# Kernel tuning notes

Hardware: AMD Instinct MI355X
Metric: run time of the kernel (lower is better)

## Reference

```python
import jax, jax.numpy as jnp
from jax import lax
import numpy as np

CHUNK = 64      # chunk_size init kwarg
MAX_LOG = 20.0  # clamp bound used in ssd()
DT_BIAS = 0.01
NEG_SLOPE = 0.01  # torch LeakyReLU default


def segsum(a):
    """a: (..., T) -> (..., T, T); ss[i,j] = sum_{k=j+1..i} a[k], -inf above diag."""
    T = a.shape[-1]
    rep = jnp.broadcast_to(a[..., :, None], a.shape + (T,))
    strict_lower = jnp.tril(jnp.ones((T, T), dtype=bool), -1)
    ss = jnp.cumsum(jnp.where(strict_lower, rep, 0.0), axis=-2)
    keep = jnp.tril(jnp.ones((T, T), dtype=bool), 0)
    return jnp.where(keep, ss, -jnp.inf)


def setup_inputs() -> dict:
    key = jax.random.key(0)
    ks = jax.random.split(key, 7)
    T, B, S, F = 4096, 4, 16, 64   # time, batch, spatial heads, in_channels
    N, P, K = 16, 64, 5            # state_dim, head_dim, conv_size
    CH = 2 * N + P + 1             # bc_conv out channels = 97
    return {
        "x": jax.random.normal(ks[0], (T, B, S, F), dtype=jnp.float32),
        "conv_w": jax.random.normal(ks[1], (CH, F, K), dtype=jnp.float32) * 0.05,
        "conv_b": jax.random.normal(ks[2], (CH,), dtype=jnp.float32) * 0.05,
        "pass_w": jax.random.normal(ks[3], (1, F), dtype=jnp.float32) * 0.1,
        "pass_b": jax.random.normal(ks[4], (1,), dtype=jnp.float32) * 0.1,
        "red_w": jax.random.normal(ks[5], (1, P), dtype=jnp.float32) * 0.1,
        "red_b": jax.random.normal(ks[6], (1,), dtype=jnp.float32) * 0.1,
        "dt_param": jnp.zeros((1,), dtype=jnp.float32),  # torch init [0.0]
    }


def _forward(x, conv_w, conv_b, pass_w, pass_b, red_w, red_b, dt_param):
    T, B, S, F = x.shape
    CH, _, K = conv_w.shape
    P = red_w.shape[1]
    N = (CH - P - 1) // 2
    c = T // CHUNK

    # ---- _compute_ssm_params (parallel mode, causal left-pad) ----
    xr = jnp.moveaxis(x.reshape(T, B * S, F), 0, 2)          # (bs, F, T)
    xp = jnp.pad(xr, ((0, 0), (0, 0), (K - 1, 0)))           # left pad context
    bcax = lax.conv_general_dilated(
        xp, conv_w, window_strides=(1,), padding="VALID",
        dimension_numbers=("NCH", "OIH", "NCH")) + conv_b[None, :, None]
    bcax = jax.nn.sigmoid(bcax) + bcax                        # (bs, CH, T)
    bcax = bcax.reshape(B, S, CH, T)
    Bm = bcax[:, :, :N, :]                                    # (b,s,n,t)
    Cm = bcax[:, :, N:2 * N, :]                               # (b,s,n,t)
    A = -jnp.abs(bcax[:, :, 2 * N, :])                        # (b,s,t)
    Xc = bcax[:, :, 2 * N + 1:, :]                            # (b,s,p,t)
    dt = jax.nn.softplus(dt_param)[0] + DT_BIAS
    lAd = dt * A                                              # (b,s,t)
    Bd = Bm * ((jnp.exp(lAd) - 1.0) / (A + 1e-9))[:, :, None, :]
    Dx = x @ pass_w[0] + pass_b[0]                            # (t,b,s) passthrough

    # ---- ssd: chunked Mamba-2 scan ----
    Xb = jnp.moveaxis(Xc, 3, 0).swapaxes(0, 1).reshape(B, c, CHUNK, S, P)
    Bb = jnp.moveaxis(Bd, 3, 0).swapaxes(0, 1).reshape(B, c, CHUNK, S, N)
    Cb = jnp.moveaxis(Cm, 3, 0).swapaxes(0, 1).reshape(B, c, CHUNK, S, N)
    Ab = lAd.reshape(B, S, c, CHUNK)                          # (b,s,c,l)
    A_cumsum = jnp.cumsum(Ab, axis=-1)                        # (b,s,c,l)

    L = jnp.exp(jnp.clip(segsum(Ab), -MAX_LOG, MAX_LOG))      # (b,s,c,l,l)
    Y_diag = jnp.einsum("bclsn,bcmsn,bsclm,bcmsp->bclsp", Cb, Bb, L, Xb)

    decay_states = jnp.exp(jnp.clip(A_cumsum[..., -1:] - A_cumsum, -MAX_LOG, MAX_LOG))
    states = jnp.einsum("bclsn,bscl,bclsp->bcspn", Bb, decay_states, Xb)
    states = jnp.concatenate([jnp.zeros_like(states[:, :1]), states], axis=1)

    A_last = jnp.pad(A_cumsum[..., -1], ((0, 0), (0, 0), (1, 0)))  # (b,s,c+1)
    decay_chunk = jnp.exp(jnp.clip(segsum(A_last), -MAX_LOG, MAX_LOG))
    new_states = jnp.einsum("bszc,bcspn->bzspn", decay_chunk, states)
    states_c = new_states[:, :-1]                             # (b,c,s,p,n)

    state_decay_out = jnp.exp(A_cumsum)                       # (b,s,c,l), no clamp (as in source)
    Y_off = jnp.einsum("bclsn,bcspn,bscl->bclsp", Cb, states_c, state_decay_out)

    Y = (Y_diag + Y_off).reshape(B, T, S, P).swapaxes(0, 1)   # (t,b,s,p)

    # ---- reduce + leaky-relu passthrough ----
    y = Y @ red_w[0] + red_b[0]                               # (t,b,s)
    return y + jnp.where(Dx >= 0, Dx, NEG_SLOPE * Dx)


def reference(x, conv_w, conv_b, pass_w, pass_b, red_w, red_b, dt_param):
    return _forward(x, conv_w, conv_b, pass_w, pass_b, red_w, red_b, dt_param)
```

## Files before the change

### kernel.cpp

```cpp
#include <hip/hip_runtime.h>
#include <hip/hip_bf16.h>
#include <math.h>


#define Tn 4096
#define BSn 64
#define Fn 64
#define CHn 97
#define CHP 112
#define Kn 5
#define Nn 16
#define NCn 64

typedef __attribute__((ext_vector_type(8))) short bf16x8;
typedef __attribute__((ext_vector_type(4))) float f32x4;

static __device__ __forceinline__ unsigned short f2bf(float v) {
    __hip_bfloat16 b = __float2bfloat16(v);
    return *reinterpret_cast<unsigned short*>(&b);
}
static __device__ __forceinline__ float bf2f(unsigned short u) {
    unsigned v = ((unsigned)u) << 16;
    return __builtin_bit_cast(float, v);
}

#define OFF_BD   0
#define OFF_CM   (OFF_BD + 4194304)
#define OFF_LAD  (OFF_CM + 4194304)
#define OFF_XQ   (OFF_LAD + 262144)
#define OFF_DL   (OFF_XQ + 262144)
#define OFF_ACS  (OFF_DL + 262144)
#define OFF_SRED (OFF_ACS + 262144)
#define OFF_CSUM (OFF_SRED + 65536)
#define OFF_SNS  (OFF_CSUM + 4096)
#define OFF_WBH  (OFF_SNS + 65536)
#define OFF_WBL  (OFF_WBH + 17920)

__global__ __launch_bounds__(256) void k_prep(const float* __restrict__ conv_w,
                                              const float* __restrict__ pass_w,
                                              unsigned short* __restrict__ wbh,
                                              unsigned short* __restrict__ wbl) {
    int idx = blockIdx.x * 256 + threadIdx.x;
    if (idx >= Kn * CHP * Fn) return;
    int f = idx & 63;
    int rest = idx >> 6;
    int ch = rest % CHP;
    int k = rest / CHP;
    float w = 0.f;
    if (ch < CHn) w = conv_w[(ch * Fn + f) * Kn + k];
    else if (ch == 97 && k == 4) w = pass_w[f];
    unsigned short hi = f2bf(w);
    wbh[idx] = hi;
    if (ch >= 32 && ch < 48)
        wbl[(k * 16 + (ch - 32)) * 64 + f] = f2bf(w - bf2f(hi));
}

__global__ __launch_bounds__(256) void k_fwd(
    const float* __restrict__ x, const unsigned short* __restrict__ wbh,
    const unsigned short* __restrict__ wbl,
    const float* __restrict__ conv_b, const float* __restrict__ pass_b,
    const float* __restrict__ red_w, const float* __restrict__ red_b,
    const float* __restrict__ dtp,
    float* __restrict__ Cm_t, float* __restrict__ Acs_ws,
    float* __restrict__ yp_ws, float* __restrict__ sred_ws,
    float* __restrict__ csum_ws) {
    const int ci = blockIdx.x, bs = blockIdx.y;
    const int tid = threadIdx.x;
    const int wv = tid >> 6, lane = tid & 63;
    const int qd = lane >> 4, n = lane & 15;

    __shared__ alignas(16) unsigned char pool[19584];
    unsigned short* xsb = (unsigned short*)pool;
    unsigned short* xlo = (unsigned short*)(pool + 9792);
    float* B0  = (float*)pool;
    float* Ct  = (float*)(pool + 5120);
    float* pxl = (float*)(pool + 10240);
    float* px2 = (float*)(pool + 11264);
    float* zsh = (float*)(pool + 12288);
    float* dl  = (float*)(pool + 12544);

    const int tB = (wv == 3) ? 6 : wv + 4;
    const unsigned short* pBw = (wv == 2) ? wbl : wbh;
    const int sB = (wv == 2) ? 16 : CHP;
    const int cB = (wv == 2) ? 0 : 16 * tB;
    bf16x8 wA[10], wB[10];
#pragma unroll
    for (int s = 0; s < 10; ++s) {
        const int k = s >> 1, f0 = 32 * (s & 1) + qd * 8;
        wA[s] = *(const bf16x8*)&wbh[((k * CHP + 16 * wv + n) << 6) + f0];
        wB[s] = *(const bf16x8*)&pBw[((k * sB + cB + n) << 6) + f0];
    }

    float4 v[5];
#pragma unroll
    for (int it = 0; it < 5; ++it) {
        int idx = tid + it * 256;
        int tt = idx >> 4, fq = (idx & 15) * 4;
        int t = ci * 64 - 4 + tt;
        v[it] = (idx < 68 * 16 && t >= 0)
                    ? *(const float4*)&x[(t * 64 + bs) * 64 + fq]
                    : make_float4(0.f, 0.f, 0.f, 0.f);
    }
#pragma unroll
    for (int it = 0; it < 5; ++it) {
        int idx = tid + it * 256;
        if (idx < 68 * 16) {
            int tt = idx >> 4, fq = (idx & 15) * 4;
            ushort4 h, lo;
            h.x = f2bf(v[it].x); lo.x = f2bf(v[it].x - bf2f(h.x));
            h.y = f2bf(v[it].y); lo.y = f2bf(v[it].y - bf2f(h.y));
            h.z = f2bf(v[it].z); lo.z = f2bf(v[it].z - bf2f(h.z));
            h.w = f2bf(v[it].w); lo.w = f2bf(v[it].w - bf2f(h.w));
            *(ushort4*)&xsb[tt * 72 + fq] = h;
            *(ushort4*)&xlo[tt * 72 + fq] = lo;
        }
    }
    __syncthreads();

    f32x4 accA[4], accB[4];
#pragma unroll
    for (int rg = 0; rg < 4; ++rg) {
        accA[rg] = (f32x4){0.f, 0.f, 0.f, 0.f};
        accB[rg] = (f32x4){0.f, 0.f, 0.f, 0.f};
    }
    if (wv == 2) {
#pragma unroll
        for (int s = 0; s < 10; ++s) {
            const int k = s >> 1, f0 = 32 * (s & 1) + qd * 8;
#pragma unroll
            for (int rg = 0; rg < 4; ++rg) {
                bf16x8 av = *(const bf16x8*)&xsb[(16 * rg + n + k) * 72 + f0];
                bf16x8 al = *(const bf16x8*)&xlo[(16 * rg + n + k) * 72 + f0];
                accA[rg] = __builtin_amdgcn_mfma_f32_16x16x32_bf16(av, wA[s], accA[rg], 0, 0, 0);
                accA[rg] = __builtin_amdgcn_mfma_f32_16x16x32_bf16(al, wA[s], accA[rg], 0, 0, 0);
                accA[rg] = __builtin_amdgcn_mfma_f32_16x16x32_bf16(av, wB[s], accA[rg], 0, 0, 0);
            }
        }
    } else {
#pragma unroll
        for (int s = 0; s < 10; ++s) {
            const int k = s >> 1, f0 = 32 * (s & 1) + qd * 8;
#pragma unroll
            for (int rg = 0; rg < 4; ++rg) {
                bf16x8 av = *(const bf16x8*)&xsb[(16 * rg + n + k) * 72 + f0];
                accA[rg] = __builtin_amdgcn_mfma_f32_16x16x32_bf16(av, wA[s], accA[rg], 0, 0, 0);
                accB[rg] = __builtin_amdgcn_mfma_f32_16x16x32_bf16(av, wB[s], accB[rg], 0, 0, 0);
            }
        }
    }
    __syncthreads();

    const int cbase = (bs * 64 + ci) * 64;
    float px[4][4];
#pragma unroll
    for (int rg = 0; rg < 4; ++rg)
#pragma unroll
        for (int reg = 0; reg < 4; ++reg) px[rg][reg] = 0.f;

    if (wv == 0) {
        const float cb0 = conv_b[n];
        const float cb4 = conv_b[64 + n], rw4 = red_w[31 + n];
#pragma unroll
        for (int rg = 0; rg < 4; ++rg)
#pragma unroll
            for (int reg = 0; reg < 4; ++reg) {
                int row = 16 * rg + 4 * qd + reg;
                float z0 = accA[rg][reg] + cb0;
                float a0 = z0 + 1.f / (1.f + __expf(-z0));
                accA[rg][reg] = a0;
                B0[row * 20 + n] = a0;
                float z4 = accB[rg][reg] + cb4;
                px[rg][reg] = (z4 + 1.f / (1.f + __expf(-z4))) * rw4;
            }
    } else if (wv == 1) {
        const float cb1 = conv_b[16 + n];
        const float cb5 = conv_b[80 + n], rw5 = red_w[47 + n];
#pragma unroll
        for (int rg = 0; rg < 4; ++rg)
#pragma unroll
            for (int reg = 0; reg < 4; ++reg) {
                int row = 16 * rg + 4 * qd + reg;
                float z1 = accA[rg][reg] + cb1;
                float a1 = z1 + 1.f / (1.f + __expf(-z1));
                Ct[row * 20 + n] = a1;
                Cm_t[(cbase + row) * 16 + n] = a1;
                float z5 = accB[rg][reg] + cb5;
                px[rg][reg] = (z5 + 1.f / (1.f + __expf(-z5))) * rw5;
            }
    } else if (wv == 2) {
        const float cb2 = conv_b[32 + n];
        const float rw2 = (n >= 1) ? red_w[n - 1] : 0.f;
#pragma unroll
        for (int rg = 0; rg < 4; ++rg)
#pragma unroll
            for (int reg = 0; reg < 4; ++reg) {
                int row = 16 * rg + 4 * qd + reg;
                if (n == 0) zsh[row] = accA[rg][reg];
                float z = accA[rg][reg] + cb2;
                px[rg][reg] = (z + 1.f / (1.f + __expf(-z))) * rw2;
            }
    } else {
        const float cb3 = conv_b[48 + n], rw3 = red_w[15 + n];
        const float cb6 = conv_b[96], rw6 = red_w[63];
        const float pb = pass_b[0], rb = red_b[0];
#pragma unroll
        for (int rg = 0; rg < 4; ++rg)
#pragma unroll
            for (int reg = 0; reg < 4; ++reg) {
                int row = 16 * rg + 4 * qd + reg;
                float z3 = accA[rg][reg] + cb3;
                px[rg][reg] = (z3 + 1.f / (1.f + __expf(-z3))) * rw3;
                if (n == 0) {
                    float z6 = accB[rg][reg] + cb6;
                    px[rg][reg] += (z6 + 1.f / (1.f + __expf(-z6))) * rw6;
                }
                if (n == 1) {
                    float Dx = accB[rg][reg] + pb;
                    float DL = (Dx >= 0.f) ? Dx : 0.01f * Dx;
                    dl[row] = DL + rb;
                }
            }
    }
#pragma unroll
    for (int m = 1; m < 16; m <<= 1)
#pragma unroll
        for (int rg = 0; rg < 4; ++rg)
#pragma unroll
            for (int reg = 0; reg < 4; ++reg)
                px[rg][reg] += __shfl_xor(px[rg][reg], m, 64);
    if (n == 0)
#pragma unroll
        for (int rg = 0; rg < 4; ++rg)
#pragma unroll
            for (int reg = 0; reg < 4; ++reg)
                pxl[wv * 64 + 16 * rg + 4 * qd + reg] = px[rg][reg];
    __syncthreads();

    const int l = lane;
    const float dt = log1pf(expf(dtp[0])) + 0.01f;
    float zA = zsh[l] + conv_b[32];
    float aA = zA + 1.f / (1.f + __expf(-zA));
    float An = -fabsf(aA);
    float lAd = dt * An;
    float fac = (__expf(lAd) - 1.f) / (An + 1e-9f);
    float s = lAd;
#pragma unroll
    for (int k = 1; k < 64; k <<= 1) {
        float t = __shfl_up(s, k, 64);
        if (l >= k) s += t;
    }
    const float acs_l = s;
    const float tot = __shfl(s, 63, 64);
    float xq = pxl[0 * 64 + l] + pxl[1 * 64 + l] + pxl[2 * 64 + l] + pxl[3 * 64 + l];
    const float wd = fac * xq;
    const float wsd = wd * __expf(fmaxf(tot - acs_l, -20.f));
    if (wv == 3) {
        Acs_ws[bs * Tn + ci * 64 + l] = acs_l;
        if (l == 0) csum_ws[bs * 64 + ci] = tot;
    }

    const float4 cc0 = *(const float4*)&Ct[l * 20 + 0];
    const float4 cc1 = *(const float4*)&Ct[l * 20 + 4];
    const float4 cc2 = *(const float4*)&Ct[l * 20 + 8];
    const float4 cc3 = *(const float4*)&Ct[l * 20 + 12];
    float part = 0.f;
#pragma unroll
    for (int mm = 0; mm < 16; ++mm) {
        const int m = 16 * wv + mm;
        const float4 b0 = *(const float4*)&B0[m * 20 + 0];
        const float4 b1 = *(const float4*)&B0[m * 20 + 4];
        const float4 b2 = *(const float4*)&B0[m * 20 + 8];
        const float4 b3 = *(const float4*)&B0[m * 20 + 12];
        float g = cc0.x * b0.x + cc0.y * b0.y + cc0.z * b0.z + cc0.w * b0.w +
                  cc1.x * b1.x + cc1.y * b1.y + cc1.z * b1.z + cc1.w * b1.w +
                  cc2.x * b2.x + cc2.y * b2.y + cc2.z * b2.z + cc2.w * b2.w +
                  cc3.x * b3.x + cc3.y * b3.y + cc3.z * b3.z + cc3.w * b3.w;
        float am = __shfl(acs_l, m, 64);
        float wm = __shfl(wd, m, 64);
        float arg = (m <= l) ? fmaxf(acs_l - am, -20.f) : -20.f;
        part += __expf(arg) * g * wm;
    }
    px2[wv * 64 + l] = part;

    if (wv == 0) {
        float sp = 0.f;
#pragma unroll
        for (int rg = 0; rg < 4; ++rg)
#pragma unroll
            for (int reg = 0; reg < 4; ++reg)
                sp += accA[rg][reg] * __shfl(wsd, 16 * rg + 4 * qd + reg, 64);
        sp += __shfl_xor(sp, 16, 64);
        sp += __shfl_xor(sp, 32, 64);
        if (l < 16) sred_ws[(bs * 64 + ci) * 16 + l] = sp;
    }
    __syncthreads();

    if (wv == 0)
        yp_ws[bs * Tn + ci * 64 + l] =
            px2[0 * 64 + l] + px2[1 * 64 + l] + px2[2 * 64 + l] + px2[3 * 64 + l] + dl[l];
}

__global__ __launch_bounds__(256) void k_scan(const float* __restrict__ sred_ws,
                                              const float* __restrict__ csum_ws,
                                              float* __restrict__ sns_ws) {
    const int wid = blockIdx.x * 4 + (threadIdx.x >> 6);
    const int ci = threadIdx.x & 63;
    const int bs = wid >> 4, n = wid & 15;
    float s = sred_ws[(bs * 64 + ci) * 16 + n];
    float d = __expf(csum_ws[bs * 64 + ci]);
#pragma unroll
    for (int k = 1; k < 64; k <<= 1) {
        float dp = __shfl_up(d, k, 64);
        float sp = __shfl_up(s, k, 64);
        if (ci >= k) {
            s = d * sp + s;
            d = d * dp;
        }
    }
    float se = __shfl_up(s, 1, 64);
    sns_ws[(bs * 64 + ci) * 16 + n] = (ci == 0) ? 0.f : se;
}

__global__ __launch_bounds__(256) void k_out(
    const float* __restrict__ Cm_t, const float* __restrict__ Acs_ws,
    const float* __restrict__ sns_ws, const float* __restrict__ yp_ws,
    float* __restrict__ out) {
    const int bs = blockIdx.y;
    const int tid = threadIdx.x;
    const int wv = tid >> 6, l = tid & 63;
    const int ci = blockIdx.x * 4 + wv;
    __shared__ float sn[4][16];
    const int base = bs * Tn + ci * 64;

    if (l < 16) sn[wv][l] = sns_ws[(bs * 64 + ci) * 16 + l];
    const float4* crow = (const float4*)&Cm_t[((bs * 64 + ci) * 64 + l) * 16];
    float4 c0 = crow[0], c1 = crow[1], c2 = crow[2], c3 = crow[3];
    float yp = yp_ws[base + l];
    float acl = Acs_ws[base + l];
    __syncthreads();

    const float* s = sn[wv];
    float go = c0.x * s[0] + c0.y * s[1] + c0.z * s[2] + c0.w * s[3] +
               c1.x * s[4] + c1.y * s[5] + c1.z * s[6] + c1.w * s[7] +
               c2.x * s[8] + c2.y * s[9] + c2.z * s[10] + c2.w * s[11] +
               c3.x * s[12] + c3.y * s[13] + c3.z * s[14] + c3.w * s[15];
    out[(ci * 64 + l) * 64 + bs] = yp + __expf(acl) * go;
}

extern "C" void kernel_launch(void* const* d_in, const int* in_sizes, int n_in,
                              void* d_out, int out_size, void* d_ws,
                              size_t ws_size, hipStream_t stream) {
    const float* x = (const float*)d_in[0];
    const float* conv_w = (const float*)d_in[1];
    const float* conv_b = (const float*)d_in[2];
    const float* pass_w = (const float*)d_in[3];
    const float* pass_b = (const float*)d_in[4];
    const float* red_w = (const float*)d_in[5];
    const float* red_b = (const float*)d_in[6];
    const float* dtp = (const float*)d_in[7];
    float* out = (float*)d_out;
    float* W = (float*)d_ws;
    (void)in_sizes; (void)n_in; (void)out_size; (void)ws_size;

    float* Cm_t = W + OFF_CM;
    float* yp_ws = W + OFF_DL;
    float* Acs_ws = W + OFF_ACS;
    float* sred_ws = W + OFF_SRED;
    float* csum_ws = W + OFF_CSUM;
    float* sns_ws = W + OFF_SNS;
    unsigned short* wbh = (unsigned short*)(W + OFF_WBH);
    unsigned short* wbl = (unsigned short*)(W + OFF_WBL);

    k_prep<<<dim3((Kn * CHP * Fn + 255) / 256), dim3(256), 0, stream>>>(
        conv_w, pass_w, wbh, wbl);
    k_fwd<<<dim3(NCn, BSn), dim3(256), 0, stream>>>(
        x, wbh, wbl, conv_b, pass_b, red_w, red_b, dtp,
        Cm_t, Acs_ws, yp_ws, sred_ws, csum_ws);
    k_scan<<<dim3(256), dim3(256), 0, stream>>>(sred_ws, csum_ws, sns_ws);
    k_out<<<dim3(NCn / 4, BSn), dim3(256), 0, stream>>>(
        Cm_t, Acs_ws, sns_ws, yp_ws, out);
}
```

Before: 203.6 us.

## Fuse chunk-state scan into output kernel and remap forward grid ordering

Removes the separate scan kernel by having each output block recompute the inter-chunk state scan for its batch-head from the reduced states, keeping only the entries for its own chunks. This eliminates one launch and the scan's workspace write/read, at the cost of redundant scan work across blocks. The forward kernel is also switched to a 1D grid with a remapped chunk/batch index ordering to change scheduling and cache locality.

```diff
diff --git a/kernel.cpp b/kernel.cpp
--- a/kernel.cpp
+++ b/kernel.cpp
@@ -64,7 +64,10 @@
     float* __restrict__ Cm_t, float* __restrict__ Acs_ws,
     float* __restrict__ yp_ws, float* __restrict__ sred_ws,
     float* __restrict__ csum_ws) {
-    const int ci = blockIdx.x, bs = blockIdx.y;
+    const int wgid = blockIdx.x;
+    const int seq = wgid >> 3;
+    const int bs = seq & 63;
+    const int ci = ((seq >> 6) << 3) | (wgid & 7);
     const int tid = threadIdx.x;
     const int wv = tid >> 6, lane = tid & 63;
     const int qd = lane >> 4, n = lane & 15;
@@ -300,31 +303,10 @@
             px2[0 * 64 + l] + px2[1 * 64 + l] + px2[2 * 64 + l] + px2[3 * 64 + l] + dl[l];
 }
 
-__global__ __launch_bounds__(256) void k_scan(const float* __restrict__ sred_ws,
-                                              const float* __restrict__ csum_ws,
-                                              float* __restrict__ sns_ws) {
-    const int wid = blockIdx.x * 4 + (threadIdx.x >> 6);
-    const int ci = threadIdx.x & 63;
-    const int bs = wid >> 4, n = wid & 15;
-    float s = sred_ws[(bs * 64 + ci) * 16 + n];
-    float d = __expf(csum_ws[bs * 64 + ci]);
-#pragma unroll
-    for (int k = 1; k < 64; k <<= 1) {
-        float dp = __shfl_up(d, k, 64);
-        float sp = __shfl_up(s, k, 64);
-        if (ci >= k) {
-            s = d * sp + s;
-            d = d * dp;
-        }
-    }
-    float se = __shfl_up(s, 1, 64);
-    sns_ws[(bs * 64 + ci) * 16 + n] = (ci == 0) ? 0.f : se;
-}
-
 __global__ __launch_bounds__(256) void k_out(
     const float* __restrict__ Cm_t, const float* __restrict__ Acs_ws,
-    const float* __restrict__ sns_ws, const float* __restrict__ yp_ws,
-    float* __restrict__ out) {
+    const float* __restrict__ sred_ws, const float* __restrict__ csum_ws,
+    const float* __restrict__ yp_ws, float* __restrict__ out) {
     const int bs = blockIdx.y;
     const int tid = threadIdx.x;
     const int wv = tid >> 6, l = tid & 63;
@@ -332,7 +314,26 @@
     __shared__ float sn[4][16];
     const int base = bs * Tn + ci * 64;
 
-    if (l < 16) sn[wv][l] = sns_ws[(bs * 64 + ci) * 16 + l];
+    const float dexp = __expf(csum_ws[bs * 64 + l]);
+#pragma unroll
+    for (int j = 0; j < 4; ++j) {
+        const int n = 4 * wv + j;
+        float s = sred_ws[(bs * 64 + l) * 16 + n];
+        float d = dexp;
+#pragma unroll
+        for (int k = 1; k < 64; k <<= 1) {
+            float dp = __shfl_up(d, k, 64);
+            float sp = __shfl_up(s, k, 64);
+            if (l >= k) {
+                s = d * sp + s;
+                d = d * dp;
+            }
+        }
+        float se = __shfl_up(s, 1, 64);
+        float sns = (l == 0) ? 0.f : se;
+        if ((l >> 2) == blockIdx.x) sn[l & 3][n] = sns;
+    }
+
     const float4* crow = (const float4*)&Cm_t[((bs * 64 + ci) * 64 + l) * 16];
     float4 c0 = crow[0], c1 = crow[1], c2 = crow[2], c3 = crow[3];
     float yp = yp_ws[base + l];
@@ -367,16 +368,14 @@
     float* Acs_ws = W + OFF_ACS;
     float* sred_ws = W + OFF_SRED;
     float* csum_ws = W + OFF_CSUM;
-    float* sns_ws = W + OFF_SNS;
     unsigned short* wbh = (unsigned short*)(W + OFF_WBH);
     unsigned short* wbl = (unsigned short*)(W + OFF_WBL);
 
     k_prep<<<dim3((Kn * CHP * Fn + 255) / 256), dim3(256), 0, stream>>>(
         conv_w, pass_w, wbh, wbl);
-    k_fwd<<<dim3(NCn, BSn), dim3(256), 0, stream>>>(
+    k_fwd<<<dim3(NCn * BSn), dim3(256), 0, stream>>>(
         x, wbh, wbl, conv_b, pass_b, red_w, red_b, dtp,
         Cm_t, Acs_ws, yp_ws, sred_ws, csum_ws);
-    k_scan<<<dim3(256), dim3(256), 0, stream>>>(sred_ws, csum_ws, sns_ws);
     k_out<<<dim3(NCn / 4, BSn), dim3(256), 0, stream>>>(
-        Cm_t, Acs_ws, sns_ws, yp_ws, out);
-}
+        Cm_t, Acs_ws, sred_ws, csum_ws, yp_ws, out);
+}
```

Result: no change. 202.0 us (-0.8%).
